# Performance work log

Hardware: AMD Instinct MI355X
Metric: run time of the kernel (lower is better)

The kernel has to match this reference:

```python
import jax, jax.numpy as jnp
import numpy as np

LAYERS = 2
HEADS = 4
TYPE_IDX = 1  # type='logic' -> 1
HIDDEN = 256
HEAD_DIM = HIDDEN // HEADS
EPS = 1e-6


def setup_inputs() -> dict:
    key = jax.random.key(0)
    ks = jax.random.split(key, 12)
    B, S, H = 4, 2048, HIDDEN
    inputs = jax.random.normal(ks[0], (B, S, H), jnp.float32)
    graphs = jax.random.uniform(ks[1], (B, 2, S, S), jnp.float32)
    biases_batch = jax.random.normal(ks[2], (B, 2, S, S), jnp.float32)
    s_h = 1.0 / np.sqrt(H).astype(np.float32)
    s_d = 1.0 / np.sqrt(HEAD_DIM).astype(np.float32)
    gc_w = jax.random.normal(ks[3], (LAYERS, H, H), jnp.float32) * s_h
    gc_b = jnp.zeros((LAYERS, H), jnp.float32)
    attn_w = jax.random.normal(ks[4], (LAYERS, HEAD_DIM, H), jnp.float32) * s_h  # conv1 (1x1) weight
    attn_a = jax.random.normal(ks[5], (LAYERS, HEAD_DIM), jnp.float32) * s_d     # conv2_1 (1x1) weight
    ln_a = jnp.ones((H,), jnp.float32)
    ln_b = jnp.zeros((H,), jnp.float32)
    w1 = jax.random.normal(ks[6], (H, H), jnp.float32) * s_h
    w1b = jnp.zeros((H,), jnp.float32)
    w2 = jax.random.normal(ks[7], (H, H), jnp.float32) * s_h
    w2b = jnp.zeros((H,), jnp.float32)
    return dict(inputs=inputs, graphs=graphs, biases_batch=biases_batch,
                gc_w=gc_w, gc_b=gc_b, attn_w=attn_w, attn_a=attn_a,
                ln_a=ln_a, ln_b=ln_b, w1=w1, w1b=w1b, w2=w2, w2b=w2b)


def reference(inputs, graphs, biases_batch, gc_w, gc_b, attn_w, attn_a, ln_a, ln_b, w1, w1b, w2, w2b):
    adj = graphs[:, TYPE_IDX]          # [b,s,s]
    bias = biases_batch[:, TYPE_IDX]   # [b,s,s]
    x0 = inputs
    x = inputs
    for i in range(LAYERS):
        # GraphConvolution: adj @ (x @ W) + b
        mf = jnp.einsum('bij,bjh->bih', adj, x @ gc_w[i]) + gc_b[i]
        # Node_Attn_head (NOTE: original uses conv2_1 for BOTH f_1 and f_2)
        seq_fts = jnp.einsum('bsh,dh->bsd', mf, attn_w[i])      # [b,s,d]
        f = seq_fts @ attn_a[i]                                  # [b,s]
        logits = jax.nn.leaky_relu(f[:, :, None] + f[:, None, :])  # f_2^T + f_1 -> [b,s,s]
        coefs = jax.nn.softmax(logits + bias, axis=1)            # Softmax(dim=1)
        ret = jax.nn.leaky_relu(jnp.einsum('bij,bjd->bid', coefs, seq_fts))  # [b,s,d]
        # shared attention head across all HEADS -> identical outputs, concatenated
        x = jnp.tile(ret, (1, 1, HEADS)) + x
    # LayerNorm (torch.std is unbiased -> ddof=1), residual to original inputs
    mean = x.mean(-1, keepdims=True)
    std = jnp.std(x, axis=-1, keepdims=True, ddof=1)
    g = ln_a * (x - mean) / (std + EPS) + ln_b + x0
    # PositionwiseFeedForward (dropout inactive in eval)
    ff = jax.nn.relu(g @ w1.T + w1b) @ w2.T + w2b
    return ff + g
```

## Files before the change

### kernel.cpp

```cpp
#include <hip/hip_runtime.h>
#include <math.h>

#define BB 4
#define SS 2048
#define HH 256
#define DD 64
#define NLAYERS 2
#define NCH 64
#define NKY 8
#define NJY 8
#define KSL (SS/NKY)
#define JSL (SS/NJY)

#define XSC  (1.f/64.f)
#define XSCI 64.f
#define FSC  (1.f/256.f)
#define WSC  256.f

typedef _Float16 f16;
typedef f16 half8 __attribute__((ext_vector_type(8)));
typedef float f32x4 __attribute__((ext_vector_type(4)));
#define MFMA16(a, b, c) __builtin_amdgcn_mfma_f32_16x16x32_f16(a, b, c, 0, 0, 0)

__device__ __forceinline__ float lrelu(float v) { return v > 0.f ? v : 0.01f * v; }
__device__ __forceinline__ int enc(float f) { int i = __float_as_int(f); return i >= 0 ? i : (i ^ 0x7fffffff); }
__device__ __forceinline__ float dec(int k) { int i = k >= 0 ? k : (k ^ 0x7fffffff); return __int_as_float(i); }
__device__ __forceinline__ void split8(const float* v, half8& h, half8& l) {
    #pragma unroll
    for (int e = 0; e < 8; ++e) {
        f16 hh = (f16)v[e]; h[e] = hh; l[e] = (f16)((v[e] - (float)hh) * 2048.f);
    }
}

__global__ __launch_bounds__(256) void split_scale(
    const float* __restrict__ src, f16* __restrict__ dh, f16* __restrict__ dl, float scale)
{
    long i = ((long)blockIdx.x * 256 + threadIdx.x) * 8;
    float4 a = *(const float4*)&src[i];
    float4 b = *(const float4*)&src[i + 4];
    float v[8] = {a.x * scale, a.y * scale, a.z * scale, a.w * scale,
                  b.x * scale, b.y * scale, b.z * scale, b.w * scale};
    half8 h, l; split8(v, h, l);
    *(half8*)&dh[i] = h; *(half8*)&dl[i] = l;
}

__global__ __launch_bounds__(256) void prep_wy(
    const float* __restrict__ gc_w, const float* __restrict__ gc_b,
    const float* __restrict__ attn_w,
    f16* __restrict__ WysH, f16* __restrict__ WysL, float* __restrict__ by,
    const float* __restrict__ w1, const float* __restrict__ w2,
    f16* __restrict__ w1h, f16* __restrict__ w1l,
    f16* __restrict__ w2h, f16* __restrict__ w2l, int* __restrict__ FMXi)
{
    int L = blockIdx.x >> 6, d = blockIdx.x & 63;
    int h = threadIdx.x;
    const float* gw = gc_w + (long)L * HH * HH;
    const float* aw = attn_w + (long)L * DD * HH + (long)d * HH;
    float acc = 0.f;
    for (int hp = 0; hp < HH; ++hp) acc += gw[(long)h * HH + hp] * aw[hp];
    f16 hh = (f16)acc;
    WysH[((long)L * DD + d) * HH + h] = hh;
    WysL[((long)L * DD + d) * HH + h] = (f16)((acc - (float)hh) * 2048.f);
    if (h == 0) {
        float ba = 0.f;
        const float* gb = gc_b + (long)L * HH;
        for (int hp = 0; hp < HH; ++hp) ba += gb[hp] * aw[hp];
        by[L * DD + d] = ba;
    }
    int gt = blockIdx.x * 256 + h;
    #pragma unroll
    for (int p = 0; p < 4; ++p) {
        int e = gt * 4 + p;
        if (e < 65536) {
            float v = w1[e]; f16 x = (f16)v;
            w1h[e] = x; w1l[e] = (f16)((v - (float)x) * 2048.f);
        } else {
            int e2 = e - 65536;
            float v = w2[e2]; f16 x = (f16)v;
            w2h[e2] = x; w2l[e2] = (f16)((v - (float)x) * 2048.f);
        }
    }
    if (blockIdx.x == 0 && h < 2 * BB) FMXi[h] = enc(-1e30f);
}

__global__ __launch_bounds__(256) void y_mfma(
    const f16* __restrict__ xh, const f16* __restrict__ xl,
    const f16* __restrict__ WyhL, const f16* __restrict__ WylL,
    f16* __restrict__ yTh, f16* __restrict__ yTl)
{
    __shared__ float Ls[64][68];
    const int blk = blockIdx.x;
    const int b = blk >> 5, st = blk & 31;
    const long row0 = (long)b * SS + st * 64;
    const int tid = threadIdx.x;
    const int w = tid >> 6, l = tid & 63, lr = l & 15, kg = (l >> 4) * 8;
    const f16* Aph = xh + (row0 + w * 16 + lr) * HH;
    const f16* Apl = xl + (row0 + w * 16 + lr) * HH;
    f32x4 acch[4] = {}, accm[4] = {};
    for (int k0 = 0; k0 < HH; k0 += 32) {
        half8 ah = *(const half8*)(Aph + k0 + kg);
        half8 al = *(const half8*)(Apl + k0 + kg);
        #pragma unroll
        for (int dt = 0; dt < 4; ++dt) {
            long boff = (long)(dt * 16 + lr) * HH + k0 + kg;
            half8 bh = *(const half8*)(WyhL + boff);
            half8 bl = *(const half8*)(WylL + boff);
            acch[dt] = MFMA16(ah, bh, acch[dt]);
            accm[dt] = MFMA16(ah, bl, accm[dt]);
            accm[dt] = MFMA16(al, bh, accm[dt]);
        }
    }
    const int rg0 = (l >> 4) * 4;
    #pragma unroll
    for (int dt = 0; dt < 4; ++dt)
        #pragma unroll
        for (int rr = 0; rr < 4; ++rr)
            Ls[w * 16 + rg0 + rr][dt * 16 + lr] = acch[dt][rr] + accm[dt][rr] * (1.f / 2048.f);
    __syncthreads();
    int d = tid >> 2, sq = (tid & 3) * 16;
    long obase = ((long)b * DD + d) * SS + st * 64 + sq;
    float v0[8], v1[8];
    #pragma unroll
    for (int e = 0; e < 8; ++e) { v0[e] = Ls[sq + e][d]; v1[e] = Ls[sq + 8 + e][d]; }
    half8 h0, l0, h1, l1; split8(v0, h0, l0); split8(v1, h1, l1);
    *(half8*)(yTh + obase) = h0; *(half8*)(yTh + obase + 8) = h1;
    *(half8*)(yTl + obase) = l0; *(half8*)(yTl + obase + 8) = l1;
}

__global__ __launch_bounds__(256) void ftp_mfma(
    const float* __restrict__ adjB,
    const f16* __restrict__ yTh, const f16* __restrict__ yTl,
    float* __restrict__ FTP)
{
    const int b = blockIdx.z;
    const int i0 = blockIdx.x * 64;
    const int ky = blockIdx.y;
    const int tid = threadIdx.x;
    const int w = tid >> 6, l = tid & 63;
    const int lr = l & 15, kg = (l >> 4) * 8;
    const float* Arow = adjB + (long)b * 2 * SS * SS + (long)(i0 + w * 16 + lr) * SS;
    const f16* Bh = yTh + ((long)b * DD + lr) * SS;
    const f16* Bl = yTl + ((long)b * DD + lr) * SS;

    f32x4 acch[4] = {}, accm[4] = {};
    for (int ks = 0; ks < KSL; ks += 32) {
        int k = ky * KSL + ks + kg;
        float4 a0 = *(const float4*)(Arow + k);
        float4 a1 = *(const float4*)(Arow + k + 4);
        float av[8] = {a0.x, a0.y, a0.z, a0.w, a1.x, a1.y, a1.z, a1.w};
        half8 ah, al; split8(av, ah, al);
        #pragma unroll
        for (int dt = 0; dt < 4; ++dt) {
            long off = (long)dt * 16 * SS + k;
            half8 bh = *(const half8*)(Bh + off);
            half8 bl = *(const half8*)(Bl + off);
            acch[dt] = MFMA16(ah, bh, acch[dt]);
            accm[dt] = MFMA16(ah, bl, accm[dt]);
            accm[dt] = MFMA16(al, bh, accm[dt]);
        }
    }
    const int rg0 = (l >> 4) * 4;
    #pragma unroll
    for (int dt = 0; dt < 4; ++dt)
        #pragma unroll
        for (int rr = 0; rr < 4; ++rr) {
            long iD = i0 + w * 16 + rg0 + rr;
            FTP[(((long)ky * BB + b) * SS + iD) * DD + dt * 16 + lr] =
                (acch[dt][rr] + accm[dt][rr] * (1.f / 2048.f)) * XSCI;
        }
}

__global__ __launch_bounds__(256) void reduce_ft_t(
    const float* __restrict__ FTP, const float* __restrict__ byL,
    const float* __restrict__ aaL, float* __restrict__ F,
    f16* __restrict__ fTh, f16* __restrict__ fTl, int* __restrict__ fmxSlot)
{
    __shared__ float Ls[64][68];
    const int blk = blockIdx.x;
    const int b = blk >> 5, st = blk & 31;
    const int s0 = st * 64;
    const int tid = threadIdx.x;
    {
        int c4 = (tid & 15) * 4, r0 = tid >> 4;
        float4 bb4 = *(const float4*)&byL[c4];
        #pragma unroll
        for (int p = 0; p < 4; ++p) {
            int r = r0 + 16 * p;
            long rowoff = ((long)b * SS + s0 + r) * DD + c4;
            float4 v = *(const float4*)&FTP[rowoff];
            #pragma unroll
            for (int ky = 1; ky < NKY; ++ky) {
                float4 u = *(const float4*)&FTP[(long)ky * BB * SS * DD + rowoff];
                v.x += u.x; v.y += u.y; v.z += u.z; v.w += u.w;
            }
            v.x += bb4.x; v.y += bb4.y; v.z += bb4.z; v.w += bb4.w;
            *(float4*)&Ls[r][c4] = v;
        }
    }
    __syncthreads();
    {
        int r = tid >> 2, q = tid & 3;
        float dot = 0.f;
        #pragma unroll
        for (int e = 0; e < 16; ++e) dot += Ls[r][q * 16 + e] * aaL[q * 16 + e];
        dot += __shfl_xor(dot, 1, 64);
        dot += __shfl_xor(dot, 2, 64);
        if (q == 0) F[b * SS + s0 + r] = dot;
        float m = dot;
        m = fmaxf(m, __shfl_down(m, 32, 64));
        m = fmaxf(m, __shfl_down(m, 16, 64));
        m = fmaxf(m, __shfl_down(m, 8, 64));
        m = fmaxf(m, __shfl_down(m, 4, 64));
        if ((tid & 63) == 0) atomicMax(fmxSlot + b, enc(m));
    }
    int d = tid >> 2, sq = (tid & 3) * 16;
    long obase = ((long)b * DD + d) * SS + s0 + sq;
    float v0[8], v1[8];
    #pragma unroll
    for (int e = 0; e < 8; ++e) { v0[e] = Ls[sq + e][d] * FSC; v1[e] = Ls[sq + 8 + e][d] * FSC; }
    half8 h0, l0, h1, l1; split8(v0, h0, l0); split8(v1, h1, l1);
    *(half8*)(fTh + obase) = h0; *(half8*)(fTh + obase + 8) = h1;
    *(half8*)(fTl + obase) = l0; *(half8*)(fTl + obase + 8) = l1;
}

__global__ __launch_bounds__(256) void col_stats_part(
    const float* __restrict__ biasb, const float* __restrict__ f,
    const int* __restrict__ fmxSlot,
    float* __restrict__ partS, float* __restrict__ Mv)
{
    __shared__ float fs[SS / NCH];
    const int b = blockIdx.z;
    const int chunk = blockIdx.y;
    const int j0 = blockIdx.x * 1024 + threadIdx.x * 4;
    const float* bb = biasb + (long)b * 2 * SS * SS;
    const int ILEN = SS / NCH;
    const int ibase = chunk * ILEN;

    if (threadIdx.x < ILEN) fs[threadIdx.x] = f[b * SS + ibase + threadIdx.x];

    float fj[4], M[4], s[4] = {0.f, 0.f, 0.f, 0.f};
    const float fmx = dec(fmxSlot[b]);
    #pragma unroll
    for (int q = 0; q < 4; ++q) {
        fj[q] = f[b * SS + j0 + q];
        M[q] = lrelu(fmx + fj[q]) + 8.f;
    }
    __syncthreads();

    for (int ii = 0; ii < ILEN; ii += 2) {
        float fi0 = fs[ii], fi1 = fs[ii + 1];
        float4 b0 = *(const float4*)&bb[(long)(ibase + ii) * SS + j0];
        float4 b1 = *(const float4*)&bb[(long)(ibase + ii + 1) * SS + j0];
        s[0] += __expf(lrelu(fi0 + fj[0]) + b0.x - M[0]);
        s[1] += __expf(lrelu(fi0 + fj[1]) + b0.y - M[1]);
        s[2] += __expf(lrelu(fi0 + fj[2]) + b0.z - M[2]);
        s[3] += __expf(lrelu(fi0 + fj[3]) + b0.w - M[3]);
        s[0] += __expf(lrelu(fi1 + fj[0]) + b1.x - M[0]);
        s[1] += __expf(lrelu(fi1 + fj[1]) + b1.y - M[1]);
        s[2] += __expf(lrelu(fi1 + fj[2]) + b1.z - M[2]);
        s[3] += __expf(lrelu(fi1 + fj[3]) + b1.w - M[3]);
    }
    #pragma unroll
    for (int q = 0; q < 4; ++q)
        partS[((long)chunk * BB + b) * SS + j0 + q] = s[q];
    if (chunk == 0) {
        #pragma unroll
        for (int q = 0; q < 4; ++q) Mv[b * SS + j0 + q] = M[q];
    }
}

__global__ __launch_bounds__(256) void col_stats_merge(
    const float* __restrict__ partS, float* __restrict__ Sinv)
{
    int idx = blockIdx.x * 256 + threadIdx.x;
    int b = idx / SS, j = idx % SS;
    float s = 0.f;
    #pragma unroll
    for (int c = 0; c < NCH; ++c)
        s += partS[((long)c * BB + b) * SS + j];
    Sinv[idx] = 1.f / s;
}

__global__ __launch_bounds__(256) void pvp_mfma(
    const float* __restrict__ biasb, const float* __restrict__ f,
    const float* __restrict__ Mv, const float* __restrict__ Sinv,
    const f16* __restrict__ fTh, const f16* __restrict__ fTl,
    float* __restrict__ PVP)
{
    const int b = blockIdx.z;
    const int i0 = blockIdx.x * 64;
    const int jy = blockIdx.y;
    const int tid = threadIdx.x;
    const int w = tid >> 6, l = tid & 63, lr = l & 15, kg = (l >> 4) * 8;
    const int irow = i0 + w * 16 + lr;
    const float fi = f[b * SS + irow];
    const float* brow = biasb + (long)b * 2 * SS * SS + (long)irow * SS;
    const float* fb = f + b * SS;
    const float* mb = Mv + b * SS;
    const float* sb = Sinv + b * SS;
    const f16* Bh = fTh + ((long)b * DD + lr) * SS;
    const f16* Bl = fTl + ((long)b * DD + lr) * SS;

    f32x4 acch[4] = {}, accm[4] = {};
    for (int jc = 0; jc < JSL; jc += 32) {
        const int jb = jy * JSL + jc + kg;
        float4 bs0 = *(const float4*)(brow + jb);
        float4 bs1 = *(const float4*)(brow + jb + 4);
        float4 fj0 = *(const float4*)(fb + jb);
        float4 fj1 = *(const float4*)(fb + jb + 4);
        float4 mj0 = *(const float4*)(mb + jb);
        float4 mj1 = *(const float4*)(mb + jb + 4);
        float4 sj0 = *(const float4*)(sb + jb);
        float4 sj1 = *(const float4*)(sb + jb + 4);
        float wv[8];
        wv[0] = __expf(lrelu(fi + fj0.x) + bs0.x - mj0.x) * sj0.x * WSC;
        wv[1] = __expf(lrelu(fi + fj0.y) + bs0.y - mj0.y) * sj0.y * WSC;
        wv[2] = __expf(lrelu(fi + fj0.z) + bs0.z - mj0.z) * sj0.z * WSC;
        wv[3] = __expf(lrelu(fi + fj0.w) + bs0.w - mj0.w) * sj0.w * WSC;
        wv[4] = __expf(lrelu(fi + fj1.x) + bs1.x - mj1.x) * sj1.x * WSC;
        wv[5] = __expf(lrelu(fi + fj1.y) + bs1.y - mj1.y) * sj1.y * WSC;
        wv[6] = __expf(lrelu(fi + fj1.z) + bs1.z - mj1.z) * sj1.z * WSC;
        wv[7] = __expf(lrelu(fi + fj1.w) + bs1.w - mj1.w) * sj1.w * WSC;
        half8 ah, al; split8(wv, ah, al);
        #pragma unroll
        for (int dt = 0; dt < 4; ++dt) {
            long off = (long)dt * 16 * SS + jb;
            half8 bh = *(const half8*)(Bh + off);
            half8 bl = *(const half8*)(Bl + off);
            acch[dt] = MFMA16(ah, bh, acch[dt]);
            accm[dt] = MFMA16(ah, bl, accm[dt]);
            accm[dt] = MFMA16(al, bh, accm[dt]);
        }
    }
    const int rg0 = (l >> 4) * 4;
    #pragma unroll
    for (int dt = 0; dt < 4; ++dt)
        #pragma unroll
        for (int rr = 0; rr < 4; ++rr) {
            long iD = i0 + w * 16 + rg0 + rr;
            PVP[(((long)jy * BB + b) * SS + iD) * DD + dt * 16 + lr] =
                acch[dt][rr] + accm[dt][rr] * (1.f / 2048.f);
        }
}

__global__ __launch_bounds__(256) void pv_combine8(
    const float* __restrict__ PVP, const float* __restrict__ xin,
    float* __restrict__ xout, f16* __restrict__ xh, f16* __restrict__ xl,
    int writeSplit)
{
    int row = blockIdx.x * 4 + (threadIdx.x >> 6);
    int d = threadIdx.x & 63;
    float v = 0.f;
    #pragma unroll
    for (int jy = 0; jy < NJY; ++jy)
        v += PVP[((long)jy * BB * SS + row) * DD + d];
    v = lrelu(v);
    #pragma unroll
    for (int rep = 0; rep < 4; ++rep) {
        long off = (long)row * HH + rep * DD + d;
        float o = v + xin[off];
        xout[off] = o;
        if (writeSplit) {
            float sv = o * XSC;
            f16 hh = (f16)sv;
            xh[off] = hh;
            xl[off] = (f16)((sv - (float)hh) * 2048.f);
        }
    }
}

__global__ __launch_bounds__(256) void layernorm_g(
    const float* __restrict__ x, const float* __restrict__ x0,
    const float* __restrict__ lna, const float* __restrict__ lnb,
    float* __restrict__ g, f16* __restrict__ gh, f16* __restrict__ gl)
{
    __shared__ float red[8];
    long row = blockIdx.x;
    int t = threadIdx.x;
    int wave = t >> 6, lane = t & 63;
    float v = x[row * HH + t];

    float sum = v;
    #pragma unroll
    for (int off = 32; off; off >>= 1) sum += __shfl_down(sum, off, 64);
    if (lane == 0) red[wave] = sum;
    __syncthreads();
    if (t < 64) {
        float s = (lane < 4) ? red[lane] : 0.f;
        s += __shfl_down(s, 2, 64);
        s += __shfl_down(s, 1, 64);
        if (lane == 0) red[4] = s / HH;
    }
    __syncthreads();
    float mean = red[4];
    float d = v - mean;
    float sq = d * d;
    #pragma unroll
    for (int off = 32; off; off >>= 1) sq += __shfl_down(sq, off, 64);
    __syncthreads();
    if (lane == 0) red[wave] = sq;
    __syncthreads();
    if (t < 64) {
        float s = (lane < 4) ? red[lane] : 0.f;
        s += __shfl_down(s, 2, 64);
        s += __shfl_down(s, 1, 64);
        if (lane == 0) red[5] = sqrtf(s / (HH - 1));
    }
    __syncthreads();
    float stdv = red[5];
    float gv = lna[t] * d / (stdv + 1e-6f) + lnb[t] + x0[row * HH + t];
    g[row * HH + t] = gv;
    f16 hh = (f16)gv;
    gh[row * HH + t] = hh;
    gl[row * HH + t] = (f16)((gv - (float)hh) * 2048.f);
}

__global__ __launch_bounds__(256) void ffn_mfma(
    const f16* __restrict__ Ah, const f16* __restrict__ Al,
    const f16* __restrict__ Bh, const f16* __restrict__ Bl,
    const float* __restrict__ bias, const float* __restrict__ res,
    float* __restrict__ outF, f16* __restrict__ outH, f16* __restrict__ outL,
    int doRelu)
{
    __shared__ float Ls[64][68];
    const int i0 = blockIdx.x * 64, j0 = blockIdx.y * 64;
    const int tid = threadIdx.x;
    const int w = tid >> 6, l = tid & 63, lr = l & 15, kg = (l >> 4) * 8;
    const f16* Aph = Ah + ((long)i0 + w * 16 + lr) * HH;
    const f16* Apl = Al + ((long)i0 + w * 16 + lr) * HH;
    f32x4 acch[4] = {}, accm[4] = {};
    for (int k0 = 0; k0 < HH; k0 += 32) {
        half8 ah = *(const half8*)(Aph + k0 + kg);
        half8 al = *(const half8*)(Apl + k0 + kg);
        #pragma unroll
        for (int dt = 0; dt < 4; ++dt) {
            long boff = ((long)(j0 + dt * 16 + lr)) * HH + k0 + kg;
            half8 bh = *(const half8*)(Bh + boff);
            half8 bl = *(const half8*)(Bl + boff);
            acch[dt] = MFMA16(ah, bh, acch[dt]);
            accm[dt] = MFMA16(ah, bl, accm[dt]);
            accm[dt] = MFMA16(al, bh, accm[dt]);
        }
    }
    const int rg0 = (l >> 4) * 4;
    #pragma unroll
    for (int dt = 0; dt < 4; ++dt) {
        float bj = bias[j0 + dt * 16 + lr];
        #pragma unroll
        for (int rr = 0; rr < 4; ++rr) {
            float v = acch[dt][rr] + accm[dt][rr] * (1.f / 2048.f) + bj;
            if (doRelu) v = fmaxf(v, 0.f);
            Ls[w * 16 + rg0 + rr][dt * 16 + lr] = v;
        }
    }
    __syncthreads();
    int s = tid >> 2, nq = (tid & 3) * 16;
    long go = ((long)i0 + s) * HH + j0 + nq;
    if (outF) {
        #pragma unroll
        for (int q = 0; q < 4; ++q) {
            float4 v = *(float4*)&Ls[s][nq + q * 4];
            if (res) {
                float4 r = *(const float4*)&res[go + q * 4];
                v.x += r.x; v.y += r.y; v.z += r.z; v.w += r.w;
            }
            *(float4*)&outF[go + q * 4] = v;
        }
    } else {
        float v0[8], v1[8];
        #pragma unroll
        for (int e = 0; e < 8; ++e) { v0[e] = Ls[s][nq + e]; v1[e] = Ls[s][nq + 8 + e]; }
        half8 h0, l0, h1, l1; split8(v0, h0, l0); split8(v1, h1, l1);
        *(half8*)&outH[go] = h0; *(half8*)&outH[go + 8] = h1;
        *(half8*)&outL[go] = l0; *(half8*)&outL[go + 8] = l1;
    }
}

extern "C" void kernel_launch(void* const* d_in, const int* in_sizes, int n_in,
                              void* d_out, int out_size, void* d_ws, size_t ws_size,
                              hipStream_t stream)
{
    const float* inputs = (const float*)d_in[0];
    const float* graphs = (const float*)d_in[1];
    const float* biases = (const float*)d_in[2];
    const float* gc_w   = (const float*)d_in[3];
    const float* gc_b   = (const float*)d_in[4];
    const float* attn_w = (const float*)d_in[5];
    const float* attn_a = (const float*)d_in[6];
    const float* ln_a   = (const float*)d_in[7];
    const float* ln_b   = (const float*)d_in[8];
    const float* w1     = (const float*)d_in[9];
    const float* w1b    = (const float*)d_in[10];
    const float* w2     = (const float*)d_in[11];
    const float* w2b    = (const float*)d_in[12];
    float* out = (float*)d_out;

    float* ws   = (float*)d_ws;
    float* X    = ws;
    float* G    = ws + 2097152;
    float* FTPV = ws + 4194304;
    float* PTS  = ws + 8388608;
    float* F    = ws + 8912896;
    float* Mv   = ws + 8921088;
    float* Sv   = ws + 8929280;
    float* by   = ws + 8937472;
    int*   FMXi = (int*)(ws + 8937600);
    f16* WysH   = (f16*)(ws + 8937728);
    f16* WysL   = (f16*)(ws + 8954112);
    f16* yTh    = (f16*)(ws + 8970496);
    f16* yTl    = (f16*)(ws + 9232640);
    f16* fTh    = (f16*)(ws + 9494784);
    f16* fTl    = (f16*)(ws + 9756928);
    f16* xh     = (f16*)(ws + 10019072);
    f16* xl     = (f16*)(ws + 11067648);
    f16* w1h    = (f16*)(ws + 12116224);
    f16* w1l    = (f16*)(ws + 12148992);
    f16* w2h    = (f16*)(ws + 12181760);
    f16* w2l    = (f16*)(ws + 12214528);

    float* FTP = FTPV;
    float* PVP = FTPV;
    f16* gh  = (f16*)(FTPV);
    f16* gl  = (f16*)(FTPV + 1048576);
    f16* h1h = (f16*)(FTPV + 2097152);
    f16* h1l = (f16*)(FTPV + 3145728);

    const float* adjBase  = graphs + (long)SS * SS;
    const float* biasBase = biases + (long)SS * SS;

    prep_wy<<<128, 256, 0, stream>>>(gc_w, gc_b, attn_w, WysH, WysL, by,
                                     w1, w2, w1h, w1l, w2h, w2l, FMXi);
    split_scale<<<1024, 256, 0, stream>>>(inputs, xh, xl, XSC);

    for (int L = 0; L < NLAYERS; ++L) {
        y_mfma<<<128, 256, 0, stream>>>(xh, xl,
            WysH + (long)L * DD * HH, WysL + (long)L * DD * HH, yTh, yTl);
        ftp_mfma<<<dim3(32, NKY, BB), 256, 0, stream>>>(adjBase, yTh, yTl, FTP);
        reduce_ft_t<<<128, 256, 0, stream>>>(FTP, by + L * DD, attn_a + (long)L * DD,
                                             F, fTh, fTl, FMXi + L * BB);
        col_stats_part<<<dim3(2, NCH, BB), 256, 0, stream>>>(biasBase, F, FMXi + L * BB, PTS, Mv);
        col_stats_merge<<<32, 256, 0, stream>>>(PTS, Sv);
        pvp_mfma<<<dim3(32, NJY, BB), 256, 0, stream>>>(biasBase, F, Mv, Sv, fTh, fTl, PVP);
        pv_combine8<<<2048, 256, 0, stream>>>(PVP, (L == 0) ? inputs : X, X,
                                              xh, xl, (L == 0) ? 1 : 0);
    }

    layernorm_g<<<BB * SS, 256, 0, stream>>>(X, inputs, ln_a, ln_b, G, gh, gl);
    ffn_mfma<<<dim3(128, 4), 256, 0, stream>>>(gh, gl, w1h, w1l, w1b,
                                               nullptr, nullptr, h1h, h1l, 1);
    ffn_mfma<<<dim3(128, 4), 256, 0, stream>>>(h1h, h1l, w2h, w2l, w2b,
                                               G, out, nullptr, nullptr, 0);
}
```

Measured before the change: 371.7 us.

## Fuse split-K partial reductions into ftp/pvp kernels and merge column stats

```diff
diff --git a/kernel.cpp b/kernel.cpp
--- a/kernel.cpp
+++ b/kernel.cpp
@@ -7,10 +7,6 @@
 #define DD 64
 #define NLAYERS 2
 #define NCH 64
-#define NKY 8
-#define NJY 8
-#define KSL (SS/NKY)
-#define JSL (SS/NJY)
 
 #define XSC  (1.f/64.f)
 #define XSCI 64.f
@@ -19,6 +15,7 @@
 
 typedef _Float16 f16;
 typedef f16 half8 __attribute__((ext_vector_type(8)));
+typedef f16 half4 __attribute__((ext_vector_type(4)));
 typedef float f32x4 __attribute__((ext_vector_type(4)));
 #define MFMA16(a, b, c) __builtin_amdgcn_mfma_f32_16x16x32_f16(a, b, c, 0, 0, 0)
 
@@ -50,7 +47,8 @@
     f16* __restrict__ WysH, f16* __restrict__ WysL, float* __restrict__ by,
     const float* __restrict__ w1, const float* __restrict__ w2,
     f16* __restrict__ w1h, f16* __restrict__ w1l,
-    f16* __restrict__ w2h, f16* __restrict__ w2l, int* __restrict__ FMXi)
+    f16* __restrict__ w2h, f16* __restrict__ w2l,
+    int* __restrict__ FMXi, int* __restrict__ CNTi)
 {
     int L = blockIdx.x >> 6, d = blockIdx.x & 63;
     int h = threadIdx.x;
@@ -81,21 +79,21 @@
         }
     }
     if (blockIdx.x == 0 && h < 2 * BB) FMXi[h] = enc(-1e30f);
-}
-
-__global__ __launch_bounds__(256) void y_mfma(
+    if (blockIdx.x == 1 && h < 16) CNTi[h] = 0;
+}
+
+__global__ __launch_bounds__(64) void y_mfma(
     const f16* __restrict__ xh, const f16* __restrict__ xl,
     const f16* __restrict__ WyhL, const f16* __restrict__ WylL,
     f16* __restrict__ yTh, f16* __restrict__ yTl)
 {
-    __shared__ float Ls[64][68];
     const int blk = blockIdx.x;
-    const int b = blk >> 5, st = blk & 31;
-    const long row0 = (long)b * SS + st * 64;
-    const int tid = threadIdx.x;
-    const int w = tid >> 6, l = tid & 63, lr = l & 15, kg = (l >> 4) * 8;
-    const f16* Aph = xh + (row0 + w * 16 + lr) * HH;
-    const f16* Apl = xl + (row0 + w * 16 + lr) * HH;
+    const int b = blk >> 7, st = blk & 127;
+    const int s0 = st * 16;
+    const int l = threadIdx.x;
+    const int lr = l & 15, kg = (l >> 4) * 8;
+    const f16* Aph = xh + ((long)b * SS + s0 + lr) * HH;
+    const f16* Apl = xl + ((long)b * SS + s0 + lr) * HH;
     f32x4 acch[4] = {}, accm[4] = {};
     for (int k0 = 0; k0 < HH; k0 += 32) {
         half8 ah = *(const half8*)(Aph + k0 + kg);
@@ -112,39 +110,40 @@
     }
     const int rg0 = (l >> 4) * 4;
     #pragma unroll
-    for (int dt = 0; dt < 4; ++dt)
-        #pragma unroll
-        for (int rr = 0; rr < 4; ++rr)
-            Ls[w * 16 + rg0 + rr][dt * 16 + lr] = acch[dt][rr] + accm[dt][rr] * (1.f / 2048.f);
-    __syncthreads();
-    int d = tid >> 2, sq = (tid & 3) * 16;
-    long obase = ((long)b * DD + d) * SS + st * 64 + sq;
-    float v0[8], v1[8];
-    #pragma unroll
-    for (int e = 0; e < 8; ++e) { v0[e] = Ls[sq + e][d]; v1[e] = Ls[sq + 8 + e][d]; }
-    half8 h0, l0, h1, l1; split8(v0, h0, l0); split8(v1, h1, l1);
-    *(half8*)(yTh + obase) = h0; *(half8*)(yTh + obase + 8) = h1;
-    *(half8*)(yTl + obase) = l0; *(half8*)(yTl + obase + 8) = l1;
-}
-
-__global__ __launch_bounds__(256) void ftp_mfma(
+    for (int dt = 0; dt < 4; ++dt) {
+        int d = dt * 16 + lr;
+        half4 h4, l4;
+        #pragma unroll
+        for (int rr = 0; rr < 4; ++rr) {
+            float v = acch[dt][rr] + accm[dt][rr] * (1.f / 2048.f);
+            f16 hh = (f16)v; h4[rr] = hh; l4[rr] = (f16)((v - (float)hh) * 2048.f);
+        }
+        long ob = ((long)b * DD + d) * SS + s0 + rg0;
+        *(half4*)(yTh + ob) = h4;
+        *(half4*)(yTl + ob) = l4;
+    }
+}
+
+__global__ __launch_bounds__(256) void ftp_fused(
     const float* __restrict__ adjB,
     const f16* __restrict__ yTh, const f16* __restrict__ yTl,
-    float* __restrict__ FTP)
-{
-    const int b = blockIdx.z;
-    const int i0 = blockIdx.x * 64;
-    const int ky = blockIdx.y;
+    const float* __restrict__ byL, const float* __restrict__ aaL,
+    float* __restrict__ F, f16* __restrict__ fTh, f16* __restrict__ fTl,
+    int* __restrict__ fmxSlot)
+{
+    __shared__ float Ls[4][16][68];
+    __shared__ float fmaxS[16];
+    const int b = blockIdx.y;
+    const int i0 = blockIdx.x * 16;
     const int tid = threadIdx.x;
-    const int w = tid >> 6, l = tid & 63;
-    const int lr = l & 15, kg = (l >> 4) * 8;
-    const float* Arow = adjB + (long)b * 2 * SS * SS + (long)(i0 + w * 16 + lr) * SS;
+    const int w = tid >> 6, l = tid & 63, lr = l & 15, kg = (l >> 4) * 8;
+    const float* Arow = adjB + (long)b * 2 * SS * SS + (long)(i0 + lr) * SS;
     const f16* Bh = yTh + ((long)b * DD + lr) * SS;
     const f16* Bl = yTl + ((long)b * DD + lr) * SS;
 
     f32x4 acch[4] = {}, accm[4] = {};
-    for (int ks = 0; ks < KSL; ks += 32) {
-        int k = ky * KSL + ks + kg;
+    for (int ks = 0; ks < 512; ks += 32) {
+        int k = w * 512 + ks + kg;
         float4 a0 = *(const float4*)(Arow + k);
         float4 a1 = *(const float4*)(Arow + k + 4);
         float av[8] = {a0.x, a0.y, a0.z, a0.w, a1.x, a1.y, a1.z, a1.w};
@@ -163,72 +162,56 @@
     #pragma unroll
     for (int dt = 0; dt < 4; ++dt)
         #pragma unroll
-        for (int rr = 0; rr < 4; ++rr) {
-            long iD = i0 + w * 16 + rg0 + rr;
-            FTP[(((long)ky * BB + b) * SS + iD) * DD + dt * 16 + lr] =
-                (acch[dt][rr] + accm[dt][rr] * (1.f / 2048.f)) * XSCI;
-        }
-}
-
-__global__ __launch_bounds__(256) void reduce_ft_t(
-    const float* __restrict__ FTP, const float* __restrict__ byL,
-    const float* __restrict__ aaL, float* __restrict__ F,
-    f16* __restrict__ fTh, f16* __restrict__ fTl, int* __restrict__ fmxSlot)
-{
-    __shared__ float Ls[64][68];
-    const int blk = blockIdx.x;
-    const int b = blk >> 5, st = blk & 31;
-    const int s0 = st * 64;
-    const int tid = threadIdx.x;
+        for (int rr = 0; rr < 4; ++rr)
+            Ls[w][rg0 + rr][dt * 16 + lr] = acch[dt][rr] + accm[dt][rr] * (1.f / 2048.f);
+    __syncthreads();
+
     {
-        int c4 = (tid & 15) * 4, r0 = tid >> 4;
-        float4 bb4 = *(const float4*)&byL[c4];
-        #pragma unroll
-        for (int p = 0; p < 4; ++p) {
-            int r = r0 + 16 * p;
-            long rowoff = ((long)b * SS + s0 + r) * DD + c4;
-            float4 v = *(const float4*)&FTP[rowoff];
-            #pragma unroll
-            for (int ky = 1; ky < NKY; ++ky) {
-                float4 u = *(const float4*)&FTP[(long)ky * BB * SS * DD + rowoff];
-                v.x += u.x; v.y += u.y; v.z += u.z; v.w += u.w;
-            }
-            v.x += bb4.x; v.y += bb4.y; v.z += bb4.z; v.w += bb4.w;
-            *(float4*)&Ls[r][c4] = v;
-        }
-    }
-    __syncthreads();
-    {
-        int r = tid >> 2, q = tid & 3;
-        float dot = 0.f;
-        #pragma unroll
-        for (int e = 0; e < 16; ++e) dot += Ls[r][q * 16 + e] * aaL[q * 16 + e];
+        int r = tid >> 4, q = tid & 15, c0 = q * 4;
+        float4 by4 = *(const float4*)&byL[c0];
+        float4 aa4 = *(const float4*)&aaL[c0];
+        float4 s;
+        s.x = (Ls[0][r][c0+0] + Ls[1][r][c0+0] + Ls[2][r][c0+0] + Ls[3][r][c0+0]) * XSCI + by4.x;
+        s.y = (Ls[0][r][c0+1] + Ls[1][r][c0+1] + Ls[2][r][c0+1] + Ls[3][r][c0+1]) * XSCI + by4.y;
+        s.z = (Ls[0][r][c0+2] + Ls[1][r][c0+2] + Ls[2][r][c0+2] + Ls[3][r][c0+2]) * XSCI + by4.z;
+        s.w = (Ls[0][r][c0+3] + Ls[1][r][c0+3] + Ls[2][r][c0+3] + Ls[3][r][c0+3]) * XSCI + by4.w;
+        *(float4*)&Ls[0][r][c0] = s;
+        float dot = s.x * aa4.x + s.y * aa4.y + s.z * aa4.z + s.w * aa4.w;
         dot += __shfl_xor(dot, 1, 64);
         dot += __shfl_xor(dot, 2, 64);
-        if (q == 0) F[b * SS + s0 + r] = dot;
-        float m = dot;
-        m = fmaxf(m, __shfl_down(m, 32, 64));
-        m = fmaxf(m, __shfl_down(m, 16, 64));
-        m = fmaxf(m, __shfl_down(m, 8, 64));
-        m = fmaxf(m, __shfl_down(m, 4, 64));
-        if ((tid & 63) == 0) atomicMax(fmxSlot + b, enc(m));
-    }
-    int d = tid >> 2, sq = (tid & 3) * 16;
-    long obase = ((long)b * DD + d) * SS + s0 + sq;
-    float v0[8], v1[8];
-    #pragma unroll
-    for (int e = 0; e < 8; ++e) { v0[e] = Ls[sq + e][d] * FSC; v1[e] = Ls[sq + 8 + e][d] * FSC; }
-    half8 h0, l0, h1, l1; split8(v0, h0, l0); split8(v1, h1, l1);
-    *(half8*)(fTh + obase) = h0; *(half8*)(fTh + obase + 8) = h1;
-    *(half8*)(fTl + obase) = l0; *(half8*)(fTl + obase + 8) = l1;
+        dot += __shfl_xor(dot, 4, 64);
+        dot += __shfl_xor(dot, 8, 64);
+        if (q == 0) { F[b * SS + i0 + r] = dot; fmaxS[r] = dot; }
+    }
+    __syncthreads();
+    if (tid == 0) {
+        float m = -1e30f;
+        #pragma unroll
+        for (int r = 0; r < 16; ++r) m = fmaxf(m, fmaxS[r]);
+        atomicMax(fmxSlot + b, enc(m));
+    }
+    {
+        int d = tid >> 2, sq = (tid & 3) * 4;
+        half4 h4, l4;
+        #pragma unroll
+        for (int e = 0; e < 4; ++e) {
+            float v = Ls[0][sq + e][d] * FSC;
+            f16 hh = (f16)v; h4[e] = hh; l4[e] = (f16)((v - (float)hh) * 2048.f);
+        }
+        long ob = ((long)b * DD + d) * SS + i0 + sq;
+        *(half4*)(fTh + ob) = h4;
+        *(half4*)(fTl + ob) = l4;
+    }
 }
 
 __global__ __launch_bounds__(256) void col_stats_part(
     const float* __restrict__ biasb, const float* __restrict__ f,
     const int* __restrict__ fmxSlot,
-    float* __restrict__ partS, float* __restrict__ Mv)
+    float* __restrict__ partS, float* __restrict__ Mv,
+    int* __restrict__ cnt, float* __restrict__ Sinv)
 {
     __shared__ float fs[SS / NCH];
+    __shared__ int lastS;
     const int b = blockIdx.z;
     const int chunk = blockIdx.y;
     const int j0 = blockIdx.x * 1024 + threadIdx.x * 4;
@@ -267,32 +250,36 @@
         #pragma unroll
         for (int q = 0; q < 4; ++q) Mv[b * SS + j0 + q] = M[q];
     }
-}
-
-__global__ __launch_bounds__(256) void col_stats_merge(
-    const float* __restrict__ partS, float* __restrict__ Sinv)
-{
-    int idx = blockIdx.x * 256 + threadIdx.x;
-    int b = idx / SS, j = idx % SS;
-    float s = 0.f;
-    #pragma unroll
-    for (int c = 0; c < NCH; ++c)
-        s += partS[((long)c * BB + b) * SS + j];
-    Sinv[idx] = 1.f / s;
-}
-
-__global__ __launch_bounds__(256) void pvp_mfma(
+    __threadfence();
+    if (threadIdx.x == 0) {
+        int old = atomicAdd(cnt + b * 2 + blockIdx.x, 1);
+        lastS = (old == NCH - 1) ? 1 : 0;
+    }
+    __syncthreads();
+    if (lastS) {
+        float4 acc = {0.f, 0.f, 0.f, 0.f};
+        for (int c = 0; c < NCH; ++c) {
+            float4 u = *(const float4*)&partS[((long)c * BB + b) * SS + j0];
+            acc.x += u.x; acc.y += u.y; acc.z += u.z; acc.w += u.w;
+        }
+        float4 r = {1.f / acc.x, 1.f / acc.y, 1.f / acc.z, 1.f / acc.w};
+        *(float4*)&Sinv[b * SS + j0] = r;
+    }
+}
+
+__global__ __launch_bounds__(256) void pvp_fused(
     const float* __restrict__ biasb, const float* __restrict__ f,
     const float* __restrict__ Mv, const float* __restrict__ Sinv,
     const f16* __restrict__ fTh, const f16* __restrict__ fTl,
-    float* __restrict__ PVP)
-{
-    const int b = blockIdx.z;
-    const int i0 = blockIdx.x * 64;
-    const int jy = blockIdx.y;
+    const float* __restrict__ xin, float* __restrict__ X,
+    f16* __restrict__ xh, f16* __restrict__ xl, int writeSplit)
+{
+    __shared__ float Ls[4][16][68];
+    const int b = blockIdx.y;
+    const int i0 = blockIdx.x * 16;
     const int tid = threadIdx.x;
     const int w = tid >> 6, l = tid & 63, lr = l & 15, kg = (l >> 4) * 8;
-    const int irow = i0 + w * 16 + lr;
+    const int irow = i0 + lr;
     const float fi = f[b * SS + irow];
     const float* brow = biasb + (long)b * 2 * SS * SS + (long)irow * SS;
     const float* fb = f + b * SS;
@@ -302,8 +289,8 @@
     const f16* Bl = fTl + ((long)b * DD + lr) * SS;
 
     f32x4 acch[4] = {}, accm[4] = {};
-    for (int jc = 0; jc < JSL; jc += 32) {
-        const int jb = jy * JSL + jc + kg;
+    for (int jc = 0; jc < 512; jc += 32) {
+        const int jb = w * 512 + jc + kg;
         float4 bs0 = *(const float4*)(brow + jb);
         float4 bs1 = *(const float4*)(brow + jb + 4);
         float4 fj0 = *(const float4*)(fb + jb);
@@ -336,35 +323,33 @@
     #pragma unroll
     for (int dt = 0; dt < 4; ++dt)
         #pragma unroll
-        for (int rr = 0; rr < 4; ++rr) {
-            long iD = i0 + w * 16 + rg0 + rr;
-            PVP[(((long)jy * BB + b) * SS + iD) * DD + dt * 16 + lr] =
-                acch[dt][rr] + accm[dt][rr] * (1.f / 2048.f);
-        }
-}
-
-__global__ __launch_bounds__(256) void pv_combine8(
-    const float* __restrict__ PVP, const float* __restrict__ xin,
-    float* __restrict__ xout, f16* __restrict__ xh, f16* __restrict__ xl,
-    int writeSplit)
-{
-    int row = blockIdx.x * 4 + (threadIdx.x >> 6);
-    int d = threadIdx.x & 63;
-    float v = 0.f;
-    #pragma unroll
-    for (int jy = 0; jy < NJY; ++jy)
-        v += PVP[((long)jy * BB * SS + row) * DD + d];
-    v = lrelu(v);
-    #pragma unroll
-    for (int rep = 0; rep < 4; ++rep) {
-        long off = (long)row * HH + rep * DD + d;
-        float o = v + xin[off];
-        xout[off] = o;
-        if (writeSplit) {
-            float sv = o * XSC;
-            f16 hh = (f16)sv;
-            xh[off] = hh;
-            xl[off] = (f16)((sv - (float)hh) * 2048.f);
+        for (int rr = 0; rr < 4; ++rr)
+            Ls[w][rg0 + rr][dt * 16 + lr] = acch[dt][rr] + accm[dt][rr] * (1.f / 2048.f);
+    __syncthreads();
+
+    {
+        int r = tid >> 4, dq = (tid & 15) * 4;
+        float v0 = lrelu(Ls[0][r][dq+0] + Ls[1][r][dq+0] + Ls[2][r][dq+0] + Ls[3][r][dq+0]);
+        float v1 = lrelu(Ls[0][r][dq+1] + Ls[1][r][dq+1] + Ls[2][r][dq+1] + Ls[3][r][dq+1]);
+        float v2 = lrelu(Ls[0][r][dq+2] + Ls[1][r][dq+2] + Ls[2][r][dq+2] + Ls[3][r][dq+2]);
+        float v3 = lrelu(Ls[0][r][dq+3] + Ls[1][r][dq+3] + Ls[2][r][dq+3] + Ls[3][r][dq+3]);
+        long rowoff = ((long)b * SS + i0 + r) * HH;
+        #pragma unroll
+        for (int rep = 0; rep < 4; ++rep) {
+            long off = rowoff + rep * DD + dq;
+            float4 xi = *(const float4*)&xin[off];
+            float4 o = {v0 + xi.x, v1 + xi.y, v2 + xi.z, v3 + xi.w};
+            *(float4*)&X[off] = o;
+            if (writeSplit) {
+                float sv[4] = {o.x * XSC, o.y * XSC, o.z * XSC, o.w * XSC};
+                half4 h4, l4;
+                #pragma unroll
+                for (int e = 0; e < 4; ++e) {
+                    f16 hh = (f16)sv[e]; h4[e] = hh; l4[e] = (f16)((sv[e] - (float)hh) * 2048.f);
+                }
+                *(half4*)&xh[off] = h4;
+                *(half4*)&xl[off] = l4;
+            }
         }
     }
 }
@@ -498,51 +483,48 @@
     float* ws   = (float*)d_ws;
     float* X    = ws;
     float* G    = ws + 2097152;
-    float* FTPV = ws + 4194304;
-    float* PTS  = ws + 8388608;
-    float* F    = ws + 8912896;
-    float* Mv   = ws + 8921088;
-    float* Sv   = ws + 8929280;
-    float* by   = ws + 8937472;
-    int*   FMXi = (int*)(ws + 8937600);
-    f16* WysH   = (f16*)(ws + 8937728);
-    f16* WysL   = (f16*)(ws + 8954112);
-    f16* yTh    = (f16*)(ws + 8970496);
-    f16* yTl    = (f16*)(ws + 9232640);
-    f16* fTh    = (f16*)(ws + 9494784);
-    f16* fTl    = (f16*)(ws + 9756928);
-    f16* xh     = (f16*)(ws + 10019072);
-    f16* xl     = (f16*)(ws + 11067648);
-    f16* w1h    = (f16*)(ws + 12116224);
-    f16* w1l    = (f16*)(ws + 12148992);
-    f16* w2h    = (f16*)(ws + 12181760);
-    f16* w2l    = (f16*)(ws + 12214528);
-
-    float* FTP = FTPV;
-    float* PVP = FTPV;
-    f16* gh  = (f16*)(FTPV);
-    f16* gl  = (f16*)(FTPV + 1048576);
-    f16* h1h = (f16*)(FTPV + 2097152);
-    f16* h1l = (f16*)(FTPV + 3145728);
+    float* PTS  = ws + 4194304;
+    float* F    = ws + 4718592;
+    float* Mv   = ws + 4726784;
+    float* Sv   = ws + 4734976;
+    float* by   = ws + 4743168;
+    int*   FMXi = (int*)(ws + 4743296);
+    int*   CNTi = (int*)(ws + 4743424);
+    f16* WysH   = (f16*)(ws + 4743552);
+    f16* WysL   = (f16*)(ws + 4759936);
+    f16* yTh    = (f16*)(ws + 4776320);
+    f16* yTl    = (f16*)(ws + 5038464);
+    f16* fTh    = (f16*)(ws + 5300608);
+    f16* fTl    = (f16*)(ws + 5562752);
+    f16* xh     = (f16*)(ws + 5824896);
+    f16* xl     = (f16*)(ws + 6873472);
+    f16* gh     = (f16*)(ws + 7922048);
+    f16* gl     = (f16*)(ws + 8970624);
+    f16* h1h    = (f16*)(ws + 10019200);
+    f16* h1l    = (f16*)(ws + 11067776);
+    f16* w1h    = (f16*)(ws + 12116352);
+    f16* w1l    = (f16*)(ws + 12149120);
+    f16* w2h    = (f16*)(ws + 12181888);
+    f16* w2l    = (f16*)(ws + 12214656);
 
     const float* adjBase  = graphs + (long)SS * SS;
     const float* biasBase = biases + (long)SS * SS;
 
     prep_wy<<<128, 256, 0, stream>>>(gc_w, gc_b, attn_w, WysH, WysL, by,
-                                     w1, w2, w1h, w1l, w2h, w2l, FMXi);
+                                     w1, w2, w1h, w1l, w2h, w2l, FMXi, CNTi);
     split_scale<<<1024, 256, 0, stream>>>(inputs, xh, xl, XSC);
 
     for (int L = 0; L < NLAYERS; ++L) {
-        y_mfma<<<128, 256, 0, stream>>>(xh, xl,
+        y_mfma<<<512, 64, 0, stream>>>(xh, xl,
             WysH + (long)L * DD * HH, WysL + (long)L * DD * HH, yTh, yTl);
-        ftp_mfma<<<dim3(32, NKY, BB), 256, 0, stream>>>(adjBase, yTh, yTl, FTP);
-        reduce_ft_t<<<128, 256, 0, stream>>>(FTP, by + L * DD, attn_a + (long)L * DD,
-                                             F, fTh, fTl, FMXi + L * BB);
-        col_stats_part<<<dim3(2, NCH, BB), 256, 0, stream>>>(biasBase, F, FMXi + L * BB, PTS, Mv);
-        col_stats_merge<<<32, 256, 0, stream>>>(PTS, Sv);
-        pvp_mfma<<<dim3(32, NJY, BB), 256, 0, stream>>>(biasBase, F, Mv, Sv, fTh, fTl, PVP);
-        pv_combine8<<<2048, 256, 0, stream>>>(PVP, (L == 0) ? inputs : X, X,
-                                              xh, xl, (L == 0) ? 1 : 0);
+        ftp_fused<<<dim3(128, BB), 256, 0, stream>>>(
+            adjBase, yTh, yTl, by + L * DD, attn_a + (long)L * DD,
+            F, fTh, fTl, FMXi + L * BB);
+        col_stats_part<<<dim3(2, NCH, BB), 256, 0, stream>>>(
+            biasBase, F, FMXi + L * BB, PTS, Mv, CNTi + L * 8, Sv);
+        pvp_fused<<<dim3(128, BB), 256, 0, stream>>>(
+            biasBase, F, Mv, Sv, fTh, fTl,
+            (L == 0) ? inputs : X, X, xh, xl, (L == 0) ? 1 : 0);
     }
 
     layernorm_g<<<BB * SS, 256, 0, stream>>>(X, inputs, ln_a, ln_b, G, gh, gl);
```

Result: slower. 400.8 us (+7.8%).
